# Optimization experiments

Hardware: AMD Instinct MI355X
Metric: run time of the kernel (lower is better)

The kernel has to match this reference:

```python
import jax, jax.numpy as jnp
import numpy as np

NBITS = 4
QN, QP = -(2 ** (NBITS - 1)), 2 ** (NBITS - 1) - 1  # -8, 7
NUM_HEADS = 12


def round_ste(x):
    # round_pass: straight-through estimator round
    return x + jax.lax.stop_gradient(jnp.round(x) - x)


def act3b(x, alpha, bias=0.0, signed=True):
    qn, qp = (-4.0, 3.0) if signed else (0.0, 7.0)
    return round_ste(jnp.clip((x + bias) / alpha, qn, qp))


def setup_inputs() -> dict:
    key = jax.random.key(0)
    ks = jax.random.split(key, 20)
    B, N, C, H = 32, 512, 768, NUM_HEADS
    hd = C // H
    u = lambda k, s: jax.random.uniform(k, s, jnp.float32, 0.05, 0.15)
    return {
        'x0': jax.random.normal(ks[0], (B, N, C), jnp.float32),
        'qkv_w': 0.02 * jax.random.normal(ks[1], (3 * C, C), jnp.float32),
        'qkv_alpha': u(ks[2], (3 * C,)),
        'qkv_bias': 0.02 * jax.random.normal(ks[3], (3 * C,), jnp.float32),
        'qkv_act_alpha': u(ks[4], (C,)),
        'proj_w': 0.02 * jax.random.normal(ks[5], (C, C), jnp.float32),
        'proj_alpha': u(ks[6], (C,)),
        'proj_bias': 0.02 * jax.random.normal(ks[7], (C,), jnp.float32),
        'proj_act_alpha': u(ks[8], (C,)),
        'normq_w': jax.random.uniform(ks[9], (hd,), jnp.float32, 0.8, 1.2),
        'normq_b': 0.01 * jax.random.normal(ks[10], (hd,), jnp.float32),
        'normk_w': jax.random.uniform(ks[11], (hd,), jnp.float32, 0.8, 1.2),
        'normk_b': 0.01 * jax.random.normal(ks[12], (hd,), jnp.float32),
        'qact_alpha': u(ks[13], (H,)),
        'kact_alpha': u(ks[14], (H,)),
        'vact_alpha': u(ks[15], (H,)),
        'attnact_alpha': u(ks[16], (H,)),
    }


def reference(x0, qkv_w, qkv_alpha, qkv_bias, qkv_act_alpha, proj_w, proj_alpha,
              proj_bias, proj_act_alpha, normq_w, normq_b, normk_w, normk_b,
              qact_alpha, kact_alpha, vact_alpha, attnact_alpha):
    B, N, C = x0.shape
    H = NUM_HEADS
    hd = C // H
    scale = hd ** -0.5

    # input activation quant (ActQ_v2, nbits=4)
    a_in = qkv_act_alpha.mean()
    x0_q = round_ste(jnp.clip(x0 / a_in, QN, QP))
    # kernel-wise 4-bit weight quant for qkv (no dequant here; scales folded later)
    w_q = round_ste(jnp.clip(qkv_w / qkv_alpha[:, None], QN, QP))
    qkv = x0_q @ w_q.T
    # integer-domain bias (truncated toward zero, like .int())
    qkv = qkv + jnp.trunc(qkv_bias / a_in / qkv_alpha)

    qkv = qkv.reshape(B, N, 3, H, hd).transpose(2, 0, 3, 1, 4)  # [3,B,H,N,hd]
    q0, k0, v0 = qkv[0], qkv[1], qkv[2]
    alpha3 = qkv_alpha.reshape(3, H, 1, hd)

    # fused scaled LayerNorm + 3-bit quant for q and k
    def norm_quant(x, ch_scale, nw, nb, act_a):
        xs = x * ch_scale  # [B,H,N,hd]
        centered = xs - xs.mean(-1, keepdims=True)
        std = jnp.std(xs, axis=-1, ddof=1, keepdims=True)
        return act3b(centered / (std + 1e-5), alpha=act_a / nw, bias=nb / nw)

    q2 = norm_quant(q0, alpha3[0], normq_w, normq_b, qact_alpha.mean())
    k2 = norm_quant(k0, alpha3[1], normk_w, normk_b, kact_alpha.mean())
    v2 = act3b(v0, alpha=vact_alpha.mean() / (a_in * alpha3[2]))

    # integer QK^T
    qk = jnp.einsum('bhqd,bhkd->bhqk', q2, k2)

    # base-2 softmax approximation
    div = 128.0
    sm_scale = scale * qact_alpha.mean() * kact_alpha.mean()
    e = jnp.trunc((1.0 / np.log(2)) * sm_scale * qk * div)
    attn_exp = jnp.exp2(jnp.round(e / div))
    attn = act3b(attn_exp / attn_exp.sum(-1, keepdims=True),
                 alpha=attnact_alpha.mean(), signed=False)

    # integer AV
    x1 = jnp.einsum('bhqk,bhkd->bhqd', attn, v2)
    x1 = x1.transpose(0, 2, 1, 3).reshape(B, N, C)
    x1_q = act3b(x1, alpha=proj_act_alpha.mean() / (attnact_alpha.mean() * vact_alpha.mean()))

    pw_q = round_ste(jnp.clip(proj_w / proj_alpha[:, None], QN, QP))
    out = (x1_q @ pw_q.T) * proj_alpha * proj_act_alpha.mean() + proj_bias
    return out
```

## Files before the change

kernel.cpp:

```cpp
#include <hip/hip_runtime.h>
#include <stdint.h>


#define BB 32
#define NN 512
#define CC 768
#define HH 12
#define HD 64
#define M_ROWS (BB * NN)
#define QKV_C (3 * CC)
#define KTA ((size_t)M_ROWS * 64)
#define KTB ((size_t)QKV_C * 64)
#define KTP ((size_t)CC * 64)

typedef int v4i __attribute__((ext_vector_type(4)));
typedef int v16i __attribute__((ext_vector_type(16)));

__device__ __forceinline__ float fadd(float a, float b) { return __fadd_rn(a, b); }
__device__ __forceinline__ float fmul(float a, float b) { return __fmul_rn(a, b); }
__device__ __forceinline__ float fdiv(float a, float b) { return __fdiv_rn(a, b); }
__device__ __forceinline__ float fsub(float a, float b) { return __fsub_rn(a, b); }

__device__ float np_sum_96(const float* a) {
  float r[8];
#pragma unroll
  for (int j = 0; j < 8; j++) r[j] = a[j];
  for (int i = 8; i < 96; i += 8)
#pragma unroll
    for (int j = 0; j < 8; j++) r[j] = fadd(r[j], a[i + j]);
  return fadd(fadd(fadd(r[0], r[1]), fadd(r[2], r[3])),
              fadd(fadd(r[4], r[5]), fadd(r[6], r[7])));
}

__device__ float np_mean_12(const float* a) {
  float r[8];
#pragma unroll
  for (int j = 0; j < 8; j++) r[j] = a[j];
  float res = fadd(fadd(fadd(r[0], r[1]), fadd(r[2], r[3])),
                   fadd(fadd(r[4], r[5]), fadd(r[6], r[7])));
  res = fadd(res, a[8]);
  res = fadd(res, a[9]);
  res = fadd(res, a[10]);
  res = fadd(res, a[11]);
  return fdiv(res, 12.0f);
}

__global__ void prep_kernel(const float* __restrict__ qkv_act_alpha,
                            const float* __restrict__ proj_act_alpha,
                            const float* __restrict__ qact_alpha,
                            const float* __restrict__ kact_alpha,
                            const float* __restrict__ vact_alpha,
                            const float* __restrict__ attnact_alpha,
                            const float* __restrict__ normq_w,
                            const float* __restrict__ normq_b,
                            const float* __restrict__ normk_w,
                            const float* __restrict__ normk_b,
                            const float* __restrict__ qkv_bias,
                            const float* __restrict__ qkv_alpha,
                            float* __restrict__ scal,
                            float* __restrict__ qparams,
                            float* __restrict__ biasq) {
  __shared__ float s_scal[8];
  __shared__ float chunk[16];
  int tid = threadIdx.x;
  if (tid < 8) chunk[tid] = np_sum_96(qkv_act_alpha + 96 * tid);
  else if (tid < 16) chunk[tid] = np_sum_96(proj_act_alpha + 96 * (tid - 8));
  if (tid == 16) s_scal[1] = np_mean_12(qact_alpha);
  if (tid == 17) s_scal[2] = np_mean_12(kact_alpha);
  if (tid == 18) s_scal[3] = np_mean_12(vact_alpha);
  if (tid == 19) s_scal[4] = np_mean_12(attnact_alpha);
  __syncthreads();
  if (tid == 0) {
    float s0 = fadd(fadd(chunk[0], chunk[1]), fadd(chunk[2], chunk[3]));
    float s1 = fadd(fadd(chunk[4], chunk[5]), fadd(chunk[6], chunk[7]));
    s_scal[0] = fdiv(fadd(s0, s1), 768.0f);
    float p0 = fadd(fadd(chunk[8], chunk[9]), fadd(chunk[10], chunk[11]));
    float p1 = fadd(fadd(chunk[12], chunk[13]), fadd(chunk[14], chunk[15]));
    s_scal[5] = fdiv(fadd(p0, p1), 768.0f);
  }
  __syncthreads();
  if (tid < 6) scal[tid] = s_scal[tid];
  if (tid < 64) {
    qparams[tid]       = fdiv(s_scal[1], normq_w[tid]);
    qparams[64 + tid]  = fdiv(normq_b[tid], normq_w[tid]);
    qparams[128 + tid] = fdiv(s_scal[2], normk_w[tid]);
    qparams[192 + tid] = fdiv(normk_b[tid], normk_w[tid]);
  }
  float a_in = s_scal[0];
  for (int c = tid; c < QKV_C; c += blockDim.x)
    biasq[c] = truncf(fdiv(fdiv(qkv_bias[c], a_in), qkv_alpha[c]));
}

__device__ __forceinline__ size_t fragaddr(int row, int b) {
  return (size_t)(row & ~31) * 64 + ((b >> 4) * 512 + (row & 31) * 16 + (b & 15));
}

__global__ void quant_x0_kernel(const float* __restrict__ x0,
                                const float* __restrict__ scal,
                                int8_t* __restrict__ x0q, int total4) {
  int i = blockIdx.x * blockDim.x + threadIdx.x;
  if (i >= total4) return;
  float a_in = scal[0];
  float4 v = ((const float4*)x0)[i];
  char4 o;
  o.x = (int8_t)rintf(fminf(fmaxf(fdiv(v.x, a_in), -8.f), 7.f));
  o.y = (int8_t)rintf(fminf(fmaxf(fdiv(v.y, a_in), -8.f), 7.f));
  o.z = (int8_t)rintf(fminf(fmaxf(fdiv(v.z, a_in), -8.f), 7.f));
  o.w = (int8_t)rintf(fminf(fmaxf(fdiv(v.w, a_in), -8.f), 7.f));
  int seq = i / 192;
  int kp = (i - seq * 192) * 4;
  int b = kp & 63;
  *(char4*)(x0q + (size_t)(kp >> 6) * KTA + fragaddr(seq, b)) = o;
}

__global__ void quant_w_kernel(const float* __restrict__ w,
                               const float* __restrict__ alpha,
                               int8_t* __restrict__ wq, int rows, int total) {
  int i = blockIdx.x * blockDim.x + threadIdx.x;
  if (i >= total) return;
  int row = i / CC;
  int k = i - row * CC;
  float t = fminf(fmaxf(fdiv(w[i], alpha[row]), -8.f), 7.f);
  wq[(size_t)(k >> 6) * ((size_t)rows * 64) + fragaddr(row, k)] =
      (int8_t)rintf(t);
}

__global__ __launch_bounds__(256, 5) void gemm_qkv_kernel(
    const int8_t* __restrict__ Aq, const int8_t* __restrict__ Wq,
    const float* __restrict__ biasq, const float* __restrict__ scal,
    const float* __restrict__ qkv_alpha, const float* __restrict__ qparams,
    int8_t* __restrict__ q2, int8_t* __restrict__ k2,
    int8_t* __restrict__ v2f) {
  __shared__ __align__(16) int8_t packT[4][3072];

  const int L = blockIdx.x;
  const int xcd = L & 7, s = L >> 3;
  const int rb = xcd + 8 * (s / 36);
  const int g = s % 36;
  const int tid = threadIdx.x;
  const int w = tid >> 6, lane = tid & 63;
  const int l31 = lane & 31, hi = lane >> 5;
  const int sec = g / HH, head = g % HH;
  const int col0 = g * 64;
  const int b_idx = rb >> 2, nbase = (rb & 3) * 128;
  const int w32 = w * 32;
  const size_t bh = (size_t)b_idx * HH + head;

  v16i acc0 = (v16i)(0), acc1 = (v16i)(0);

  const int8_t* pa = Aq + (size_t)(rb * 128 + w32) * 64 + hi * 512 + l31 * 16;
  const int8_t* pb = Wq + (size_t)col0 * 64 + hi * 512 + l31 * 16;

  if (sec < 2) {
    v4i Aa = *(const v4i*)(pa);
    v4i Ab = *(const v4i*)(pa + 1024);
    v4i B0a = *(const v4i*)(pb);
    v4i B0b = *(const v4i*)(pb + 1024);
    v4i B1a = *(const v4i*)(pb + 2048);
    v4i B1b = *(const v4i*)(pb + 3072);
#pragma unroll 1
    for (int kt = 0; kt < 11; kt++) {
      const int8_t* npa = pa + (size_t)(kt + 1) * KTA;
      const int8_t* npb = pb + (size_t)(kt + 1) * KTB;
      v4i nAa = *(const v4i*)(npa);
      v4i nAb = *(const v4i*)(npa + 1024);
      v4i nB0a = *(const v4i*)(npb);
      v4i nB0b = *(const v4i*)(npb + 1024);
      v4i nB1a = *(const v4i*)(npb + 2048);
      v4i nB1b = *(const v4i*)(npb + 3072);
      acc0 = __builtin_amdgcn_mfma_i32_32x32x32_i8(B0a, Aa, acc0, 0, 0, 0);
      acc1 = __builtin_amdgcn_mfma_i32_32x32x32_i8(B1a, Aa, acc1, 0, 0, 0);
      acc0 = __builtin_amdgcn_mfma_i32_32x32x32_i8(B0b, Ab, acc0, 0, 0, 0);
      acc1 = __builtin_amdgcn_mfma_i32_32x32x32_i8(B1b, Ab, acc1, 0, 0, 0);
      Aa = nAa; Ab = nAb; B0a = nB0a; B0b = nB0b; B1a = nB1a; B1b = nB1b;
    }
    acc0 = __builtin_amdgcn_mfma_i32_32x32x32_i8(B0a, Aa, acc0, 0, 0, 0);
    acc1 = __builtin_amdgcn_mfma_i32_32x32x32_i8(B1a, Aa, acc1, 0, 0, 0);
    acc0 = __builtin_amdgcn_mfma_i32_32x32x32_i8(B0b, Ab, acc0, 0, 0, 0);
    acc1 = __builtin_amdgcn_mfma_i32_32x32x32_i8(B1b, Ab, acc1, 0, 0, 0);
    float xs[2][16];
#pragma unroll
    for (int i = 0; i < 2; i++)
#pragma unroll
      for (int b = 0; b < 4; b++) {
        int cg = col0 + 32 * i + 8 * b + 4 * hi;
        float4 bqv = *(const float4*)(biasq + cg);
        float4 alv = *(const float4*)(qkv_alpha + cg);
        const float* bqp = (const float*)&bqv;
        const float* alp = (const float*)&alv;
#pragma unroll
        for (int c = 0; c < 4; c++) {
          int av = (i == 0) ? acc0[4 * b + c] : acc1[4 * b + c];
          xs[i][4 * b + c] = fmul(fadd((float)av, bqp[c]), alp[c]);
        }
      }
    float rc[4];
#pragma unroll
    for (int c = 0; c < 4; c++) rc[c] = xs[0][c];
#pragma unroll
    for (int b = 1; b < 4; b++)
#pragma unroll
      for (int c = 0; c < 4; c++) rc[c] = fadd(rc[c], xs[0][4 * b + c]);
#pragma unroll
    for (int b = 0; b < 4; b++)
#pragma unroll
      for (int c = 0; c < 4; c++) rc[c] = fadd(rc[c], xs[1][4 * b + c]);
    float Ls = fadd(fadd(rc[0], rc[1]), fadd(rc[2], rc[3]));
    float Rs = __shfl_xor(Ls, 32, 64);
    float mn = fdiv(fadd(Ls, Rs), 64.0f);
    float vc[4];
#pragma unroll
    for (int c = 0; c < 4; c++) {
      float d = fsub(xs[0][c], mn);
      vc[c] = fmul(d, d);
    }
#pragma unroll
    for (int b = 1; b < 4; b++)
#pragma unroll
      for (int c = 0; c < 4; c++) {
        float d = fsub(xs[0][4 * b + c], mn);
        vc[c] = fadd(vc[c], fmul(d, d));
      }
#pragma unroll
    for (int b = 0; b < 4; b++)
#pragma unroll
      for (int c = 0; c < 4; c++) {
        float d = fsub(xs[1][4 * b + c], mn);
        vc[c] = fadd(vc[c], fmul(d, d));
      }
    float Lv = fadd(fadd(vc[0], vc[1]), fadd(vc[2], vc[3]));
    float Rv = __shfl_xor(Lv, 32, 64);
    float var = fdiv(fadd(Lv, Rv), 63.0f);
    float den = fadd(__fsqrt_rn(var), 1e-5f);
    const float* ap = qparams + (sec == 0 ? 0 : 128);
#pragma unroll
    for (int i = 0; i < 2; i++)
#pragma unroll
      for (int b = 0; b < 4; b++) {
        int cin = 32 * i + 8 * b + 4 * hi;
        float4 a4 = *(const float4*)(ap + cin);
        float4 b4 = *(const float4*)(ap + 64 + cin);
        const float* a4p = (const float*)&a4;
        const float* b4p = (const float*)&b4;
        uint32_t pk = 0;
#pragma unroll
        for (int c = 0; c < 4; c++) {
          float xn = fdiv(fsub(xs[i][4 * b + c], mn), den);
          float t = fdiv(fadd(xn, b4p[c]), a4p[c]);
          t = fminf(fmaxf(t, -4.f), 3.f);
          pk |= ((uint32_t)(uint8_t)(int8_t)rintf(t)) << (8 * c);
        }
        *(uint32_t*)&packT[w][l31 * 80 + cin] = pk;
      }
    asm volatile("s_waitcnt lgkmcnt(0)" ::: "memory");
    int8_t* dst = (sec == 0) ? q2 : k2;
    size_t rowbase = bh * NN + nbase + w32;
#pragma unroll
    for (int c = 0; c < 2; c++) {
      int id = lane + 64 * c;
      int row = id >> 2, off = (id & 3) * 16;
      int4 ov = *(const int4*)&packT[w][row * 80 + off];
      *(int4*)(dst + (rowbase + row) * 64 + off) = ov;
    }
  } else {
    v4i Aa = *(const v4i*)(pa);
    v4i Ab = *(const v4i*)(pa + 1024);
    v4i B0a = *(const v4i*)(pb);
    v4i B0b = *(const v4i*)(pb + 1024);
    v4i B1a = *(const v4i*)(pb + 2048);
    v4i B1b = *(const v4i*)(pb + 3072);
#pragma unroll 1
    for (int kt = 0; kt < 11; kt++) {
      const int8_t* npa = pa + (size_t)(kt + 1) * KTA;
      const int8_t* npb = pb + (size_t)(kt + 1) * KTB;
      v4i nAa = *(const v4i*)(npa);
      v4i nAb = *(const v4i*)(npa + 1024);
      v4i nB0a = *(const v4i*)(npb);
      v4i nB0b = *(const v4i*)(npb + 1024);
      v4i nB1a = *(const v4i*)(npb + 2048);
      v4i nB1b = *(const v4i*)(npb + 3072);
      acc0 = __builtin_amdgcn_mfma_i32_32x32x32_i8(Aa, B0a, acc0, 0, 0, 0);
      acc1 = __builtin_amdgcn_mfma_i32_32x32x32_i8(Aa, B1a, acc1, 0, 0, 0);
      acc0 = __builtin_amdgcn_mfma_i32_32x32x32_i8(Ab, B0b, acc0, 0, 0, 0);
      acc1 = __builtin_amdgcn_mfma_i32_32x32x32_i8(Ab, B1b, acc1, 0, 0, 0);
      Aa = nAa; Ab = nAb; B0a = nB0a; B0b = nB0b; B1a = nB1a; B1b = nB1b;
    }
    acc0 = __builtin_amdgcn_mfma_i32_32x32x32_i8(Aa, B0a, acc0, 0, 0, 0);
    acc1 = __builtin_amdgcn_mfma_i32_32x32x32_i8(Aa, B1a, acc1, 0, 0, 0);
    acc0 = __builtin_amdgcn_mfma_i32_32x32x32_i8(Ab, B0b, acc0, 0, 0, 0);
    acc1 = __builtin_amdgcn_mfma_i32_32x32x32_i8(Ab, B1b, acc1, 0, 0, 0);
    const float a_in = scal[0], vact = scal[3];
#pragma unroll
    for (int sj = 0; sj < 2; sj++) {
      int cg = col0 + 32 * sj + l31;
      float bq = biasq[cg];
      float va = fdiv(vact, fmul(a_in, qkv_alpha[cg]));
      int dloc = 32 * sj + l31;
#pragma unroll
      for (int b = 0; b < 4; b++) {
        uint32_t pk = 0;
#pragma unroll
        for (int c = 0; c < 4; c++) {
          int av = (sj == 0) ? acc0[4 * b + c] : acc1[4 * b + c];
          float vint = fadd((float)av, bq);
          float t = fminf(fmaxf(fdiv(vint, va), -4.f), 3.f);
          pk |= ((uint32_t)(uint8_t)(int8_t)rintf(t)) << (8 * c);
        }
        *(uint32_t*)&packT[w][dloc * 48 + 8 * b + 4 * hi] = pk;
      }
    }
    asm volatile("s_waitcnt lgkmcnt(0)" ::: "memory");
#pragma unroll
    for (int c = 0; c < 2; c++) {
      int id = lane + 64 * c;
      int row = id >> 1, off = (id & 1) * 16;
      int4 ov = *(const int4*)&packT[w][row * 48 + off];
      int n0 = nbase + w32 + off;
      *(int4*)(v2f + (size_t)bh * 32768 + ((n0 >> 6) * 4096) +
               ((row >> 4) * 1024) + ((row & 15) * 64) +
               (((n0 >> 4) & 3) * 16)) = ov;
    }
  }
}

__global__ __launch_bounds__(256) void attn_kernel(
    const int8_t* __restrict__ q2, const int8_t* __restrict__ k2,
    const int8_t* __restrict__ v2f, const float* __restrict__ scal,
    int8_t* __restrict__ x1q) {
  __shared__ __align__(16) int8_t At[64][80];

  const int L = blockIdx.x;
  const int xcd = L & 7, s = L >> 3;
  const int bh = xcd + 8 * (s >> 3);
  const int qt = s & 7;
  const int tid = threadIdx.x;
  const int w = tid >> 6, lane = tid & 63, quad = lane >> 4, c16 = lane & 15;
  const int sr = tid >> 2, scol = (tid & 3) << 4;
  const float attnm = scal[4];
  const float coef =
      fmul(1.4426950408889634f, fmul(fmul(0.125f, scal[1]), scal[2]));
  const float coef128 = fmul(coef, 128.f);
  const size_t base = (size_t)bh * NN * HD;

  const int8_t* kptr = k2 + base + (size_t)c16 * 64 + quad * 16;
  const int8_t* vptr = v2f + base + (size_t)c16 * 64 + quad * 16;
  v4i qf = *(const v4i*)(q2 + base + (size_t)(qt * 64 + 16 * w + c16) * 64 +
                         quad * 16);

  uint32_t mpack[8][4];
  float Srow = 0.f;
  v4i kfr[4];
#pragma unroll
  for (int f = 0; f < 4; f++)
    kfr[f] = *(const v4i*)(kptr + f * 1024);
#pragma unroll
  for (int kt = 0; kt < 8; kt++) {
    float psum = 0.f;
#pragma unroll
    for (int f = 0; f < 4; f++) {
      v4i kf = kfr[f];
      if (kt < 7)
        kfr[f] = *(const v4i*)(kptr + (kt + 1) * 4096 + f * 1024);
      v4i d2 = (v4i){0, 0, 0, 0};
      d2 = __builtin_amdgcn_mfma_i32_16x16x64_i8(kf, qf, d2, 0, 0, 0);
      uint32_t pk = 0;
#pragma unroll
      for (int r = 0; r < 4; r++) {
        float e = truncf(fmul(coef128, (float)d2[r]));
        int mi = (int)rintf(fmul(e, 0.0078125f));
        psum = fadd(psum, ldexpf(1.0f, mi));
        pk |= ((uint32_t)(uint8_t)(int8_t)mi) << (8 * r);
      }
      mpack[kt][f] = pk;
    }
    psum = fadd(psum, __shfl_xor(psum, 16, 64));
    psum = fadd(psum, __shfl_xor(psum, 32, 64));
    Srow = fadd(Srow, psum);
  }
  const float u = fdiv(fdiv(1.0f, Srow), attnm);

  v4i xacc[4];
#pragma unroll
  for (int s2 = 0; s2 < 4; s2++) xacc[s2] = (v4i){0, 0, 0, 0};
  v4i vfr[4];
#pragma unroll
  for (int s2 = 0; s2 < 4; s2++)
    vfr[s2] = *(const v4i*)(vptr + s2 * 1024);

#pragma unroll
  for (int kt = 0; kt < 8; kt++) {
#pragma unroll
    for (int f = 0; f < 4; f++) {
      uint32_t pk = mpack[kt][f];
      uint32_t wpk = 0;
#pragma unroll
      for (int r = 0; r < 4; r++) {
        int mi = (int)(int8_t)(pk >> (8 * r));
        float t = fminf(ldexpf(u, mi), 7.f);
        wpk |= ((uint32_t)(uint8_t)(int8_t)rintf(t)) << (8 * r);
      }
      *(uint32_t*)&At[16 * w + c16][16 * f + 4 * quad] = wpk;
    }
    asm volatile("s_waitcnt lgkmcnt(0)" ::: "memory");
    v4i af = *(const v4i*)&At[16 * w + c16][quad * 16];
#pragma unroll
    for (int s2 = 0; s2 < 4; s2++) {
      v4i vf = vfr[s2];
      if (kt < 7)
        vfr[s2] = *(const v4i*)(vptr + (kt + 1) * 4096 + s2 * 1024);
      xacc[s2] = __builtin_amdgcn_mfma_i32_16x16x64_i8(vf, af, xacc[s2], 0, 0, 0);
    }
  }

  const float pa = fdiv(scal[5], fmul(attnm, scal[3]));
#pragma unroll
  for (int s2 = 0; s2 < 4; s2++) {
    uint32_t pack = 0;
#pragma unroll
    for (int r = 0; r < 4; r++) {
      float t = fminf(fmaxf(fdiv((float)xacc[s2][r], pa), -4.f), 3.f);
      pack |= ((uint32_t)(uint8_t)(int8_t)rintf(t)) << (8 * r);
    }
    *(uint32_t*)&At[16 * w + c16][16 * s2 + 4 * quad] = pack;
  }
  __syncthreads();
  int4 ov = *(const int4*)&At[sr][scol];
  *(int4*)(x1q + ((size_t)bh * NN + qt * 64 + sr) * HD + scol) = ov;
}

__global__ __launch_bounds__(256, 5) void gemm_proj_kernel(
    const int8_t* __restrict__ x1q, const int8_t* __restrict__ Wq,
    const float* __restrict__ proj_alpha, const float* __restrict__ proj_bias,
    const float* __restrict__ scal, float* __restrict__ out) {
  const int L = blockIdx.x;
  const int xcd = L & 7, s = L >> 3;
  const int rb = xcd + 8 * (s / 12);
  const int g = s % 12;
  const int tid = threadIdx.x;
  const int w = tid >> 6, lane = tid & 63;
  const int l31 = lane & 31, hi = lane >> 5;
  const int col0 = g * 64;
  const int b_idx = rb >> 2, nbase = (rb & 3) * 128;
  const int w32 = w * 32;

  v16i acc0 = (v16i)(0), acc1 = (v16i)(0);

  const int8_t* pa =
      x1q + ((size_t)b_idx * HH * NN + nbase + w32 + l31) * 64 + hi * 16;
  const int8_t* pb = Wq + (size_t)col0 * 64 + hi * 512 + l31 * 16;
  const size_t KTX = (size_t)NN * 64;

  v4i Aa = *(const v4i*)(pa);
  v4i Ab = *(const v4i*)(pa + 32);
  v4i B0a = *(const v4i*)(pb);
  v4i B0b = *(const v4i*)(pb + 1024);
  v4i B1a = *(const v4i*)(pb + 2048);
  v4i B1b = *(const v4i*)(pb + 3072);
#pragma unroll 1
  for (int kt = 0; kt < 11; kt++) {
    const int8_t* npa = pa + (size_t)(kt + 1) * KTX;
    const int8_t* npb = pb + (size_t)(kt + 1) * KTP;
    v4i nAa = *(const v4i*)(npa);
    v4i nAb = *(const v4i*)(npa + 32);
    v4i nB0a = *(const v4i*)(npb);
    v4i nB0b = *(const v4i*)(npb + 1024);
    v4i nB1a = *(const v4i*)(npb + 2048);
    v4i nB1b = *(const v4i*)(npb + 3072);
    acc0 = __builtin_amdgcn_mfma_i32_32x32x32_i8(B0a, Aa, acc0, 0, 0, 0);
    acc1 = __builtin_amdgcn_mfma_i32_32x32x32_i8(B1a, Aa, acc1, 0, 0, 0);
    acc0 = __builtin_amdgcn_mfma_i32_32x32x32_i8(B0b, Ab, acc0, 0, 0, 0);
    acc1 = __builtin_amdgcn_mfma_i32_32x32x32_i8(B1b, Ab, acc1, 0, 0, 0);
    Aa = nAa; Ab = nAb; B0a = nB0a; B0b = nB0b; B1a = nB1a; B1b = nB1b;
  }
  acc0 = __builtin_amdgcn_mfma_i32_32x32x32_i8(B0a, Aa, acc0, 0, 0, 0);
  acc1 = __builtin_amdgcn_mfma_i32_32x32x32_i8(B1a, Aa, acc1, 0, 0, 0);
  acc0 = __builtin_amdgcn_mfma_i32_32x32x32_i8(B0b, Ab, acc0, 0, 0, 0);
  acc1 = __builtin_amdgcn_mfma_i32_32x32x32_i8(B1b, Ab, acc1, 0, 0, 0);

  const float pact = scal[5];
  const int m = rb * 128 + w32 + l31;
#pragma unroll
  for (int i = 0; i < 2; i++)
#pragma unroll
    for (int b = 0; b < 4; b++) {
      int colb = col0 + 32 * i + 8 * b + 4 * hi;
      float4 al = *(const float4*)(proj_alpha + colb);
      float4 bi = *(const float4*)(proj_bias + colb);
      const float* alp = (const float*)&al;
      const float* bip = (const float*)&bi;
      float4 o;
      float* op = (float*)&o;
#pragma unroll
      for (int c = 0; c < 4; c++) {
        int av = (i == 0) ? acc0[4 * b + c] : acc1[4 * b + c];
        op[c] = fadd(fmul(fmul((float)av, alp[c]), pact), bip[c]);
      }
      *(float4*)(out + (size_t)m * CC + colb) = o;
    }
}

extern "C" void kernel_launch(void* const* d_in, const int* in_sizes, int n_in,
                              void* d_out, int out_size, void* d_ws,
                              size_t ws_size, hipStream_t stream) {
  const float* x0 = (const float*)d_in[0];
  const float* qkv_w = (const float*)d_in[1];
  const float* qkv_alpha = (const float*)d_in[2];
  const float* qkv_bias = (const float*)d_in[3];
  const float* qkv_act_alpha = (const float*)d_in[4];
  const float* proj_w = (const float*)d_in[5];
  const float* proj_alpha = (const float*)d_in[6];
  const float* proj_bias = (const float*)d_in[7];
  const float* proj_act_alpha = (const float*)d_in[8];
  const float* normq_w = (const float*)d_in[9];
  const float* normq_b = (const float*)d_in[10];
  const float* normk_w = (const float*)d_in[11];
  const float* normk_b = (const float*)d_in[12];
  const float* qact_alpha = (const float*)d_in[13];
  const float* kact_alpha = (const float*)d_in[14];
  const float* vact_alpha = (const float*)d_in[15];
  const float* attnact_alpha = (const float*)d_in[16];

  char* ws = (char*)d_ws;
  size_t off = 0;
  auto alloc = [&](size_t bytes) -> char* {
    char* p = ws + off;
    off += (bytes + 255) & ~(size_t)255;
    return p;
  };
  float* scal = (float*)alloc(64 * 4);
  float* qparams = (float*)alloc(256 * 4);
  float* biasq = (float*)alloc(QKV_C * 4);
  int8_t* x0q = (int8_t*)alloc((size_t)M_ROWS * CC);
  int8_t* wq = (int8_t*)alloc((size_t)QKV_C * CC);
  int8_t* pwq = (int8_t*)alloc((size_t)CC * CC);
  int8_t* q2 = (int8_t*)alloc((size_t)BB * HH * NN * HD);
  int8_t* k2 = (int8_t*)alloc((size_t)BB * HH * NN * HD);
  int8_t* v2f = (int8_t*)alloc((size_t)BB * HH * NN * HD);
  int8_t* x1q = (int8_t*)alloc((size_t)M_ROWS * CC);

  prep_kernel<<<1, 256, 0, stream>>>(qkv_act_alpha, proj_act_alpha, qact_alpha,
                                     kact_alpha, vact_alpha, attnact_alpha,
                                     normq_w, normq_b, normk_w, normk_b,
                                     qkv_bias, qkv_alpha, scal, qparams, biasq);

  int total4 = M_ROWS * CC / 4;
  quant_x0_kernel<<<(total4 + 255) / 256, 256, 0, stream>>>(x0, scal, x0q,
                                                            total4);
  quant_w_kernel<<<(QKV_C * CC + 255) / 256, 256, 0, stream>>>(
      qkv_w, qkv_alpha, wq, QKV_C, QKV_C * CC);
  quant_w_kernel<<<(CC * CC + 255) / 256, 256, 0, stream>>>(
      proj_w, proj_alpha, pwq, CC, CC * CC);

  gemm_qkv_kernel<<<36 * (M_ROWS / 128), 256, 0, stream>>>(
      x0q, wq, biasq, scal, qkv_alpha, qparams, q2, k2, v2f);

  attn_kernel<<<(NN / 64) * (BB * HH), 256, 0, stream>>>(q2, k2, v2f, scal,
                                                         x1q);

  gemm_proj_kernel<<<12 * (M_ROWS / 128), 256, 0, stream>>>(
      x1q, pwq, proj_alpha, proj_bias, scal, (float*)d_out);
}
```

Measured before the change: 298.5 us.

## Double the row tile per wave in both int8 GEMMs to 64x64

Each wave in the QKV and projection GEMMs now computes a 64-row by 64-column tile with four MFMA accumulators instead of 32x64 with two. Each B fragment is reused across two A fragments, which cuts global B loads per MFMA, and the grids shrink by half to match. The epilogues loop over the two row halves. In exchange, register pressure roughly doubles, so the occupancy hint of 5 is dropped and fewer workgroups can be resident. The smaller grid may also reduce load balance across CUs.

```diff
diff --git a/kernel.cpp b/kernel.cpp
--- a/kernel.cpp
+++ b/kernel.cpp
@@ -125,7 +125,7 @@
       (int8_t)rintf(t);
 }
 
-__global__ __launch_bounds__(256, 5) void gemm_qkv_kernel(
+__global__ __launch_bounds__(256) void gemm_qkv_kernel(
     const int8_t* __restrict__ Aq, const int8_t* __restrict__ Wq,
     const float* __restrict__ biasq, const float* __restrict__ scal,
     const float* __restrict__ qkv_alpha, const float* __restrict__ qparams,
@@ -142,18 +142,21 @@
   const int l31 = lane & 31, hi = lane >> 5;
   const int sec = g / HH, head = g % HH;
   const int col0 = g * 64;
-  const int b_idx = rb >> 2, nbase = (rb & 3) * 128;
-  const int w32 = w * 32;
+  const int b_idx = rb >> 1, nbase = (rb & 1) * 256;
+  const int w64 = w * 64;
   const size_t bh = (size_t)b_idx * HH + head;
 
-  v16i acc0 = (v16i)(0), acc1 = (v16i)(0);
-
-  const int8_t* pa = Aq + (size_t)(rb * 128 + w32) * 64 + hi * 512 + l31 * 16;
+  v16i acc00 = (v16i)(0), acc01 = (v16i)(0);
+  v16i acc10 = (v16i)(0), acc11 = (v16i)(0);
+
+  const int8_t* pa = Aq + (size_t)(rb * 256 + w64) * 64 + hi * 512 + l31 * 16;
   const int8_t* pb = Wq + (size_t)col0 * 64 + hi * 512 + l31 * 16;
 
   if (sec < 2) {
-    v4i Aa = *(const v4i*)(pa);
-    v4i Ab = *(const v4i*)(pa + 1024);
+    v4i A0a = *(const v4i*)(pa);
+    v4i A0b = *(const v4i*)(pa + 1024);
+    v4i A1a = *(const v4i*)(pa + 2048);
+    v4i A1b = *(const v4i*)(pa + 3072);
     v4i B0a = *(const v4i*)(pb);
     v4i B0b = *(const v4i*)(pb + 1024);
     v4i B1a = *(const v4i*)(pb + 2048);
@@ -162,109 +165,130 @@
     for (int kt = 0; kt < 11; kt++) {
       const int8_t* npa = pa + (size_t)(kt + 1) * KTA;
       const int8_t* npb = pb + (size_t)(kt + 1) * KTB;
-      v4i nAa = *(const v4i*)(npa);
-      v4i nAb = *(const v4i*)(npa + 1024);
+      v4i nA0a = *(const v4i*)(npa);
+      v4i nA0b = *(const v4i*)(npa + 1024);
+      v4i nA1a = *(const v4i*)(npa + 2048);
+      v4i nA1b = *(const v4i*)(npa + 3072);
       v4i nB0a = *(const v4i*)(npb);
       v4i nB0b = *(const v4i*)(npb + 1024);
       v4i nB1a = *(const v4i*)(npb + 2048);
       v4i nB1b = *(const v4i*)(npb + 3072);
-      acc0 = __builtin_amdgcn_mfma_i32_32x32x32_i8(B0a, Aa, acc0, 0, 0, 0);
-      acc1 = __builtin_amdgcn_mfma_i32_32x32x32_i8(B1a, Aa, acc1, 0, 0, 0);
-      acc0 = __builtin_amdgcn_mfma_i32_32x32x32_i8(B0b, Ab, acc0, 0, 0, 0);
-      acc1 = __builtin_amdgcn_mfma_i32_32x32x32_i8(B1b, Ab, acc1, 0, 0, 0);
-      Aa = nAa; Ab = nAb; B0a = nB0a; B0b = nB0b; B1a = nB1a; B1b = nB1b;
-    }
-    acc0 = __builtin_amdgcn_mfma_i32_32x32x32_i8(B0a, Aa, acc0, 0, 0, 0);
-    acc1 = __builtin_amdgcn_mfma_i32_32x32x32_i8(B1a, Aa, acc1, 0, 0, 0);
-    acc0 = __builtin_amdgcn_mfma_i32_32x32x32_i8(B0b, Ab, acc0, 0, 0, 0);
-    acc1 = __builtin_amdgcn_mfma_i32_32x32x32_i8(B1b, Ab, acc1, 0, 0, 0);
-    float xs[2][16];
-#pragma unroll
-    for (int i = 0; i < 2; i++)
-#pragma unroll
-      for (int b = 0; b < 4; b++) {
-        int cg = col0 + 32 * i + 8 * b + 4 * hi;
-        float4 bqv = *(const float4*)(biasq + cg);
-        float4 alv = *(const float4*)(qkv_alpha + cg);
-        const float* bqp = (const float*)&bqv;
-        const float* alp = (const float*)&alv;
+      acc00 = __builtin_amdgcn_mfma_i32_32x32x32_i8(B0a, A0a, acc00, 0, 0, 0);
+      acc01 = __builtin_amdgcn_mfma_i32_32x32x32_i8(B1a, A0a, acc01, 0, 0, 0);
+      acc10 = __builtin_amdgcn_mfma_i32_32x32x32_i8(B0a, A1a, acc10, 0, 0, 0);
+      acc11 = __builtin_amdgcn_mfma_i32_32x32x32_i8(B1a, A1a, acc11, 0, 0, 0);
+      acc00 = __builtin_amdgcn_mfma_i32_32x32x32_i8(B0b, A0b, acc00, 0, 0, 0);
+      acc01 = __builtin_amdgcn_mfma_i32_32x32x32_i8(B1b, A0b, acc01, 0, 0, 0);
+      acc10 = __builtin_amdgcn_mfma_i32_32x32x32_i8(B0b, A1b, acc10, 0, 0, 0);
+      acc11 = __builtin_amdgcn_mfma_i32_32x32x32_i8(B1b, A1b, acc11, 0, 0, 0);
+      A0a = nA0a; A0b = nA0b; A1a = nA1a; A1b = nA1b;
+      B0a = nB0a; B0b = nB0b; B1a = nB1a; B1b = nB1b;
+    }
+    acc00 = __builtin_amdgcn_mfma_i32_32x32x32_i8(B0a, A0a, acc00, 0, 0, 0);
+    acc01 = __builtin_amdgcn_mfma_i32_32x32x32_i8(B1a, A0a, acc01, 0, 0, 0);
+    acc10 = __builtin_amdgcn_mfma_i32_32x32x32_i8(B0a, A1a, acc10, 0, 0, 0);
+    acc11 = __builtin_amdgcn_mfma_i32_32x32x32_i8(B1a, A1a, acc11, 0, 0, 0);
+    acc00 = __builtin_amdgcn_mfma_i32_32x32x32_i8(B0b, A0b, acc00, 0, 0, 0);
+    acc01 = __builtin_amdgcn_mfma_i32_32x32x32_i8(B1b, A0b, acc01, 0, 0, 0);
+    acc10 = __builtin_amdgcn_mfma_i32_32x32x32_i8(B0b, A1b, acc10, 0, 0, 0);
+    acc11 = __builtin_amdgcn_mfma_i32_32x32x32_i8(B1b, A1b, acc11, 0, 0, 0);
+
+    const float* ap = qparams + (sec == 0 ? 0 : 128);
+    int8_t* dst = (sec == 0) ? q2 : k2;
+#pragma unroll
+    for (int p = 0; p < 2; p++) {
+      float xs[2][16];
+#pragma unroll
+      for (int i = 0; i < 2; i++)
+#pragma unroll
+        for (int b = 0; b < 4; b++) {
+          int cg = col0 + 32 * i + 8 * b + 4 * hi;
+          float4 bqv = *(const float4*)(biasq + cg);
+          float4 alv = *(const float4*)(qkv_alpha + cg);
+          const float* bqp = (const float*)&bqv;
+          const float* alp = (const float*)&alv;
+#pragma unroll
+          for (int c = 0; c < 4; c++) {
+            int av;
+            if (p == 0)
+              av = (i == 0) ? acc00[4 * b + c] : acc01[4 * b + c];
+            else
+              av = (i == 0) ? acc10[4 * b + c] : acc11[4 * b + c];
+            xs[i][4 * b + c] = fmul(fadd((float)av, bqp[c]), alp[c]);
+          }
+        }
+      float rc[4];
+#pragma unroll
+      for (int c = 0; c < 4; c++) rc[c] = xs[0][c];
+#pragma unroll
+      for (int b = 1; b < 4; b++)
+#pragma unroll
+        for (int c = 0; c < 4; c++) rc[c] = fadd(rc[c], xs[0][4 * b + c]);
+#pragma unroll
+      for (int b = 0; b < 4; b++)
+#pragma unroll
+        for (int c = 0; c < 4; c++) rc[c] = fadd(rc[c], xs[1][4 * b + c]);
+      float Ls = fadd(fadd(rc[0], rc[1]), fadd(rc[2], rc[3]));
+      float Rs = __shfl_xor(Ls, 32, 64);
+      float mn = fdiv(fadd(Ls, Rs), 64.0f);
+      float vc[4];
+#pragma unroll
+      for (int c = 0; c < 4; c++) {
+        float d = fsub(xs[0][c], mn);
+        vc[c] = fmul(d, d);
+      }
+#pragma unroll
+      for (int b = 1; b < 4; b++)
 #pragma unroll
         for (int c = 0; c < 4; c++) {
-          int av = (i == 0) ? acc0[4 * b + c] : acc1[4 * b + c];
-          xs[i][4 * b + c] = fmul(fadd((float)av, bqp[c]), alp[c]);
+          float d = fsub(xs[0][4 * b + c], mn);
+          vc[c] = fadd(vc[c], fmul(d, d));
         }
+#pragma unroll
+      for (int b = 0; b < 4; b++)
+#pragma unroll
+        for (int c = 0; c < 4; c++) {
+          float d = fsub(xs[1][4 * b + c], mn);
+          vc[c] = fadd(vc[c], fmul(d, d));
+        }
+      float Lv = fadd(fadd(vc[0], vc[1]), fadd(vc[2], vc[3]));
+      float Rv = __shfl_xor(Lv, 32, 64);
+      float var = fdiv(fadd(Lv, Rv), 63.0f);
+      float den = fadd(__fsqrt_rn(var), 1e-5f);
+#pragma unroll
+      for (int i = 0; i < 2; i++)
+#pragma unroll
+        for (int b = 0; b < 4; b++) {
+          int cin = 32 * i + 8 * b + 4 * hi;
+          float4 a4 = *(const float4*)(ap + cin);
+          float4 b4 = *(const float4*)(ap + 64 + cin);
+          const float* a4p = (const float*)&a4;
+          const float* b4p = (const float*)&b4;
+          uint32_t pk = 0;
+#pragma unroll
+          for (int c = 0; c < 4; c++) {
+            float xn = fdiv(fsub(xs[i][4 * b + c], mn), den);
+            float t = fdiv(fadd(xn, b4p[c]), a4p[c]);
+            t = fminf(fmaxf(t, -4.f), 3.f);
+            pk |= ((uint32_t)(uint8_t)(int8_t)rintf(t)) << (8 * c);
+          }
+          *(uint32_t*)&packT[w][l31 * 80 + cin] = pk;
+        }
+      asm volatile("s_waitcnt lgkmcnt(0)" ::: "memory");
+      size_t rowbase = bh * NN + nbase + w64 + p * 32;
+#pragma unroll
+      for (int c = 0; c < 2; c++) {
+        int id = lane + 64 * c;
+        int row = id >> 2, off = (id & 3) * 16;
+        int4 ov = *(const int4*)&packT[w][row * 80 + off];
+        *(int4*)(dst + (rowbase + row) * 64 + off) = ov;
       }
-    float rc[4];
-#pragma unroll
-    for (int c = 0; c < 4; c++) rc[c] = xs[0][c];
-#pragma unroll
-    for (int b = 1; b < 4; b++)
-#pragma unroll
-      for (int c = 0; c < 4; c++) rc[c] = fadd(rc[c], xs[0][4 * b + c]);
-#pragma unroll
-    for (int b = 0; b < 4; b++)
-#pragma unroll
-      for (int c = 0; c < 4; c++) rc[c] = fadd(rc[c], xs[1][4 * b + c]);
-    float Ls = fadd(fadd(rc[0], rc[1]), fadd(rc[2], rc[3]));
-    float Rs = __shfl_xor(Ls, 32, 64);
-    float mn = fdiv(fadd(Ls, Rs), 64.0f);
-    float vc[4];
-#pragma unroll
-    for (int c = 0; c < 4; c++) {
-      float d = fsub(xs[0][c], mn);
-      vc[c] = fmul(d, d);
-    }
-#pragma unroll
-    for (int b = 1; b < 4; b++)
-#pragma unroll
-      for (int c = 0; c < 4; c++) {
-        float d = fsub(xs[0][4 * b + c], mn);
-        vc[c] = fadd(vc[c], fmul(d, d));
-      }
-#pragma unroll
-    for (int b = 0; b < 4; b++)
-#pragma unroll
-      for (int c = 0; c < 4; c++) {
-        float d = fsub(xs[1][4 * b + c], mn);
-        vc[c] = fadd(vc[c], fmul(d, d));
-      }
-    float Lv = fadd(fadd(vc[0], vc[1]), fadd(vc[2], vc[3]));
-    float Rv = __shfl_xor(Lv, 32, 64);
-    float var = fdiv(fadd(Lv, Rv), 63.0f);
-    float den = fadd(__fsqrt_rn(var), 1e-5f);
-    const float* ap = qparams + (sec == 0 ? 0 : 128);
-#pragma unroll
-    for (int i = 0; i < 2; i++)
-#pragma unroll
-      for (int b = 0; b < 4; b++) {
-        int cin = 32 * i + 8 * b + 4 * hi;
-        float4 a4 = *(const float4*)(ap + cin);
-        float4 b4 = *(const float4*)(ap + 64 + cin);
-        const float* a4p = (const float*)&a4;
-        const float* b4p = (const float*)&b4;
-        uint32_t pk = 0;
-#pragma unroll
-        for (int c = 0; c < 4; c++) {
-          float xn = fdiv(fsub(xs[i][4 * b + c], mn), den);
-          float t = fdiv(fadd(xn, b4p[c]), a4p[c]);
-          t = fminf(fmaxf(t, -4.f), 3.f);
-          pk |= ((uint32_t)(uint8_t)(int8_t)rintf(t)) << (8 * c);
-        }
-        *(uint32_t*)&packT[w][l31 * 80 + cin] = pk;
-      }
-    asm volatile("s_waitcnt lgkmcnt(0)" ::: "memory");
-    int8_t* dst = (sec == 0) ? q2 : k2;
-    size_t rowbase = bh * NN + nbase + w32;
-#pragma unroll
-    for (int c = 0; c < 2; c++) {
-      int id = lane + 64 * c;
-      int row = id >> 2, off = (id & 3) * 16;
-      int4 ov = *(const int4*)&packT[w][row * 80 + off];
-      *(int4*)(dst + (rowbase + row) * 64 + off) = ov;
     }
   } else {
-    v4i Aa = *(const v4i*)(pa);
-    v4i Ab = *(const v4i*)(pa + 1024);
+    v4i A0a = *(const v4i*)(pa);
+    v4i A0b = *(const v4i*)(pa + 1024);
+    v4i A1a = *(const v4i*)(pa + 2048);
+    v4i A1b = *(const v4i*)(pa + 3072);
     v4i B0a = *(const v4i*)(pb);
     v4i B0b = *(const v4i*)(pb + 1024);
     v4i B1a = *(const v4i*)(pb + 2048);
@@ -273,52 +297,71 @@
     for (int kt = 0; kt < 11; kt++) {
       const int8_t* npa = pa + (size_t)(kt + 1) * KTA;
       const int8_t* npb = pb + (size_t)(kt + 1) * KTB;
-      v4i nAa = *(const v4i*)(npa);
-      v4i nAb = *(const v4i*)(npa + 1024);
+      v4i nA0a = *(const v4i*)(npa);
+      v4i nA0b = *(const v4i*)(npa + 1024);
+      v4i nA1a = *(const v4i*)(npa + 2048);
+      v4i nA1b = *(const v4i*)(npa + 3072);
       v4i nB0a = *(const v4i*)(npb);
       v4i nB0b = *(const v4i*)(npb + 1024);
       v4i nB1a = *(const v4i*)(npb + 2048);
       v4i nB1b = *(const v4i*)(npb + 3072);
-      acc0 = __builtin_amdgcn_mfma_i32_32x32x32_i8(Aa, B0a, acc0, 0, 0, 0);
-      acc1 = __builtin_amdgcn_mfma_i32_32x32x32_i8(Aa, B1a, acc1, 0, 0, 0);
-      acc0 = __builtin_amdgcn_mfma_i32_32x32x32_i8(Ab, B0b, acc0, 0, 0, 0);
-      acc1 = __builtin_amdgcn_mfma_i32_32x32x32_i8(Ab, B1b, acc1, 0, 0, 0);
-      Aa = nAa; Ab = nAb; B0a = nB0a; B0b = nB0b; B1a = nB1a; B1b = nB1b;
-    }
-    acc0 = __builtin_amdgcn_mfma_i32_32x32x32_i8(Aa, B0a, acc0, 0, 0, 0);
-    acc1 = __builtin_amdgcn_mfma_i32_32x32x32_i8(Aa, B1a, acc1, 0, 0, 0);
-    acc0 = __builtin_amdgcn_mfma_i32_32x32x32_i8(Ab, B0b, acc0, 0, 0, 0);
-    acc1 = __builtin_amdgcn_mfma_i32_32x32x32_i8(Ab, B1b, acc1, 0, 0, 0);
+      acc00 = __builtin_amdgcn_mfma_i32_32x32x32_i8(A0a, B0a, acc00, 0, 0, 0);
+      acc01 = __builtin_amdgcn_mfma_i32_32x32x32_i8(A0a, B1a, acc01, 0, 0, 0);
+      acc10 = __builtin_amdgcn_mfma_i32_32x32x32_i8(A1a, B0a, acc10, 0, 0, 0);
+      acc11 = __builtin_amdgcn_mfma_i32_32x32x32_i8(A1a, B1a, acc11, 0, 0, 0);
+      acc00 = __builtin_amdgcn_mfma_i32_32x32x32_i8(A0b, B0b, acc00, 0, 0, 0);
+      acc01 = __builtin_amdgcn_mfma_i32_32x32x32_i8(A0b, B1b, acc01, 0, 0, 0);
+      acc10 = __builtin_amdgcn_mfma_i32_32x32x32_i8(A1b, B0b, acc10, 0, 0, 0);
+      acc11 = __builtin_amdgcn_mfma_i32_32x32x32_i8(A1b, B1b, acc11, 0, 0, 0);
+      A0a = nA0a; A0b = nA0b; A1a = nA1a; A1b = nA1b;
+      B0a = nB0a; B0b = nB0b; B1a = nB1a; B1b = nB1b;
+    }
+    acc00 = __builtin_amdgcn_mfma_i32_32x32x32_i8(A0a, B0a, acc00, 0, 0, 0);
+    acc01 = __builtin_amdgcn_mfma_i32_32x32x32_i8(A0a, B1a, acc01, 0, 0, 0);
+    acc10 = __builtin_amdgcn_mfma_i32_32x32x32_i8(A1a, B0a, acc10, 0, 0, 0);
+    acc11 = __builtin_amdgcn_mfma_i32_32x32x32_i8(A1a, B1a, acc11, 0, 0, 0);
+    acc00 = __builtin_amdgcn_mfma_i32_32x32x32_i8(A0b, B0b, acc00, 0, 0, 0);
+    acc01 = __builtin_amdgcn_mfma_i32_32x32x32_i8(A0b, B1b, acc01, 0, 0, 0);
+    acc10 = __builtin_amdgcn_mfma_i32_32x32x32_i8(A1b, B0b, acc10, 0, 0, 0);
+    acc11 = __builtin_amdgcn_mfma_i32_32x32x32_i8(A1b, B1b, acc11, 0, 0, 0);
+
     const float a_in = scal[0], vact = scal[3];
 #pragma unroll
-    for (int sj = 0; sj < 2; sj++) {
-      int cg = col0 + 32 * sj + l31;
-      float bq = biasq[cg];
-      float va = fdiv(vact, fmul(a_in, qkv_alpha[cg]));
-      int dloc = 32 * sj + l31;
-#pragma unroll
-      for (int b = 0; b < 4; b++) {
-        uint32_t pk = 0;
-#pragma unroll
-        for (int c = 0; c < 4; c++) {
-          int av = (sj == 0) ? acc0[4 * b + c] : acc1[4 * b + c];
-          float vint = fadd((float)av, bq);
-          float t = fminf(fmaxf(fdiv(vint, va), -4.f), 3.f);
-          pk |= ((uint32_t)(uint8_t)(int8_t)rintf(t)) << (8 * c);
+    for (int p = 0; p < 2; p++) {
+#pragma unroll
+      for (int sj = 0; sj < 2; sj++) {
+        int cg = col0 + 32 * sj + l31;
+        float bq = biasq[cg];
+        float va = fdiv(vact, fmul(a_in, qkv_alpha[cg]));
+        int dloc = 32 * sj + l31;
+#pragma unroll
+        for (int b = 0; b < 4; b++) {
+          uint32_t pk = 0;
+#pragma unroll
+          for (int c = 0; c < 4; c++) {
+            int av;
+            if (p == 0)
+              av = (sj == 0) ? acc00[4 * b + c] : acc01[4 * b + c];
+            else
+              av = (sj == 0) ? acc10[4 * b + c] : acc11[4 * b + c];
+            float vint = fadd((float)av, bq);
+            float t = fminf(fmaxf(fdiv(vint, va), -4.f), 3.f);
+            pk |= ((uint32_t)(uint8_t)(int8_t)rintf(t)) << (8 * c);
+          }
+          *(uint32_t*)&packT[w][dloc * 48 + 8 * b + 4 * hi] = pk;
         }
-        *(uint32_t*)&packT[w][dloc * 48 + 8 * b + 4 * hi] = pk;
       }
-    }
-    asm volatile("s_waitcnt lgkmcnt(0)" ::: "memory");
-#pragma unroll
-    for (int c = 0; c < 2; c++) {
-      int id = lane + 64 * c;
-      int row = id >> 1, off = (id & 1) * 16;
-      int4 ov = *(const int4*)&packT[w][row * 48 + off];
-      int n0 = nbase + w32 + off;
-      *(int4*)(v2f + (size_t)bh * 32768 + ((n0 >> 6) * 4096) +
-               ((row >> 4) * 1024) + ((row & 15) * 64) +
-               (((n0 >> 4) & 3) * 16)) = ov;
+      asm volatile("s_waitcnt lgkmcnt(0)" ::: "memory");
+#pragma unroll
+      for (int c = 0; c < 2; c++) {
+        int id = lane + 64 * c;
+        int row = id >> 1, off = (id & 1) * 16;
+        int4 ov = *(const int4*)&packT[w][row * 48 + off];
+        int n0 = nbase + w64 + p * 32 + off;
+        *(int4*)(v2f + (size_t)bh * 32768 + ((n0 >> 6) * 4096) +
+                 ((row >> 4) * 1024) + ((row & 15) * 64) +
+                 (((n0 >> 4) & 3) * 16)) = ov;
+      }
     }
   }
 }
@@ -428,7 +471,7 @@
   *(int4*)(x1q + ((size_t)bh * NN + qt * 64 + sr) * HD + scol) = ov;
 }
 
-__global__ __launch_bounds__(256, 5) void gemm_proj_kernel(
+__global__ __launch_bounds__(256) void gemm_proj_kernel(
     const int8_t* __restrict__ x1q, const int8_t* __restrict__ Wq,
     const float* __restrict__ proj_alpha, const float* __restrict__ proj_bias,
     const float* __restrict__ scal, float* __restrict__ out) {
@@ -440,18 +483,21 @@
   const int w = tid >> 6, lane = tid & 63;
   const int l31 = lane & 31, hi = lane >> 5;
   const int col0 = g * 64;
-  const int b_idx = rb >> 2, nbase = (rb & 3) * 128;
-  const int w32 = w * 32;
-
-  v16i acc0 = (v16i)(0), acc1 = (v16i)(0);
+  const int b_idx = rb >> 1, nbase = (rb & 1) * 256;
+  const int w64 = w * 64;
+
+  v16i acc00 = (v16i)(0), acc01 = (v16i)(0);
+  v16i acc10 = (v16i)(0), acc11 = (v16i)(0);
 
   const int8_t* pa =
-      x1q + ((size_t)b_idx * HH * NN + nbase + w32 + l31) * 64 + hi * 16;
+      x1q + ((size_t)b_idx * HH * NN + nbase + w64 + l31) * 64 + hi * 16;
   const int8_t* pb = Wq + (size_t)col0 * 64 + hi * 512 + l31 * 16;
   const size_t KTX = (size_t)NN * 64;
 
-  v4i Aa = *(const v4i*)(pa);
-  v4i Ab = *(const v4i*)(pa + 32);
+  v4i A0a = *(const v4i*)(pa);
+  v4i A0b = *(const v4i*)(pa + 32);
+  v4i A1a = *(const v4i*)(pa + 2048);
+  v4i A1b = *(const v4i*)(pa + 2048 + 32);
   v4i B0a = *(const v4i*)(pb);
   v4i B0b = *(const v4i*)(pb + 1024);
   v4i B1a = *(const v4i*)(pb + 2048);
@@ -460,43 +506,61 @@
   for (int kt = 0; kt < 11; kt++) {
     const int8_t* npa = pa + (size_t)(kt + 1) * KTX;
     const int8_t* npb = pb + (size_t)(kt + 1) * KTP;
-    v4i nAa = *(const v4i*)(npa);
-    v4i nAb = *(const v4i*)(npa + 32);
+    v4i nA0a = *(const v4i*)(npa);
+    v4i nA0b = *(const v4i*)(npa + 32);
+    v4i nA1a = *(const v4i*)(npa + 2048);
+    v4i nA1b = *(const v4i*)(npa + 2048 + 32);
     v4i nB0a = *(const v4i*)(npb);
     v4i nB0b = *(const v4i*)(npb + 1024);
     v4i nB1a = *(const v4i*)(npb + 2048);
     v4i nB1b = *(const v4i*)(npb + 3072);
-    acc0 = __builtin_amdgcn_mfma_i32_32x32x32_i8(B0a, Aa, acc0, 0, 0, 0);
-    acc1 = __builtin_amdgcn_mfma_i32_32x32x32_i8(B1a, Aa, acc1, 0, 0, 0);
-    acc0 = __builtin_amdgcn_mfma_i32_32x32x32_i8(B0b, Ab, acc0, 0, 0, 0);
-    acc1 = __builtin_amdgcn_mfma_i32_32x32x32_i8(B1b, Ab, acc1, 0, 0, 0);
-    Aa = nAa; Ab = nAb; B0a = nB0a; B0b = nB0b; B1a = nB1a; B1b = nB1b;
-  }
-  acc0 = __builtin_amdgcn_mfma_i32_32x32x32_i8(B0a, Aa, acc0, 0, 0, 0);
-  acc1 = __builtin_amdgcn_mfma_i32_32x32x32_i8(B1a, Aa, acc1, 0, 0, 0);
-  acc0 = __builtin_amdgcn_mfma_i32_32x32x32_i8(B0b, Ab, acc0, 0, 0, 0);
-  acc1 = __builtin_amdgcn_mfma_i32_32x32x32_i8(B1b, Ab, acc1, 0, 0, 0);
+    acc00 = __builtin_amdgcn_mfma_i32_32x32x32_i8(B0a, A0a, acc00, 0, 0, 0);
+    acc01 = __builtin_amdgcn_mfma_i32_32x32x32_i8(B1a, A0a, acc01, 0, 0, 0);
+    acc10 = __builtin_amdgcn_mfma_i32_32x32x32_i8(B0a, A1a, acc10, 0, 0, 0);
+    acc11 = __builtin_amdgcn_mfma_i32_32x32x32_i8(B1a, A1a, acc11, 0, 0, 0);
+    acc00 = __builtin_amdgcn_mfma_i32_32x32x32_i8(B0b, A0b, acc00, 0, 0, 0);
+    acc01 = __builtin_amdgcn_mfma_i32_32x32x32_i8(B1b, A0b, acc01, 0, 0, 0);
+    acc10 = __builtin_amdgcn_mfma_i32_32x32x32_i8(B0b, A1b, acc10, 0, 0, 0);
+    acc11 = __builtin_amdgcn_mfma_i32_32x32x32_i8(B1b, A1b, acc11, 0, 0, 0);
+    A0a = nA0a; A0b = nA0b; A1a = nA1a; A1b = nA1b;
+    B0a = nB0a; B0b = nB0b; B1a = nB1a; B1b = nB1b;
+  }
+  acc00 = __builtin_amdgcn_mfma_i32_32x32x32_i8(B0a, A0a, acc00, 0, 0, 0);
+  acc01 = __builtin_amdgcn_mfma_i32_32x32x32_i8(B1a, A0a, acc01, 0, 0, 0);
+  acc10 = __builtin_amdgcn_mfma_i32_32x32x32_i8(B0a, A1a, acc10, 0, 0, 0);
+  acc11 = __builtin_amdgcn_mfma_i32_32x32x32_i8(B1a, A1a, acc11, 0, 0, 0);
+  acc00 = __builtin_amdgcn_mfma_i32_32x32x32_i8(B0b, A0b, acc00, 0, 0, 0);
+  acc01 = __builtin_amdgcn_mfma_i32_32x32x32_i8(B1b, A0b, acc01, 0, 0, 0);
+  acc10 = __builtin_amdgcn_mfma_i32_32x32x32_i8(B0b, A1b, acc10, 0, 0, 0);
+  acc11 = __builtin_amdgcn_mfma_i32_32x32x32_i8(B1b, A1b, acc11, 0, 0, 0);
 
   const float pact = scal[5];
-  const int m = rb * 128 + w32 + l31;
-#pragma unroll
-  for (int i = 0; i < 2; i++)
-#pragma unroll
-    for (int b = 0; b < 4; b++) {
-      int colb = col0 + 32 * i + 8 * b + 4 * hi;
-      float4 al = *(const float4*)(proj_alpha + colb);
-      float4 bi = *(const float4*)(proj_bias + colb);
-      const float* alp = (const float*)&al;
-      const float* bip = (const float*)&bi;
-      float4 o;
-      float* op = (float*)&o;
-#pragma unroll
-      for (int c = 0; c < 4; c++) {
-        int av = (i == 0) ? acc0[4 * b + c] : acc1[4 * b + c];
-        op[c] = fadd(fmul(fmul((float)av, alp[c]), pact), bip[c]);
+#pragma unroll
+  for (int p = 0; p < 2; p++) {
+    const int m = rb * 256 + w64 + p * 32 + l31;
+#pragma unroll
+    for (int i = 0; i < 2; i++)
+#pragma unroll
+      for (int b = 0; b < 4; b++) {
+        int colb = col0 + 32 * i + 8 * b + 4 * hi;
+        float4 al = *(const float4*)(proj_alpha + colb);
+        float4 bi = *(const float4*)(proj_bias + colb);
+        const float* alp = (const float*)&al;
+        const float* bip = (const float*)&bi;
+        float4 o;
+        float* op = (float*)&o;
+#pragma unroll
+        for (int c = 0; c < 4; c++) {
+          int av;
+          if (p == 0)
+            av = (i == 0) ? acc00[4 * b + c] : acc01[4 * b + c];
+          else
+            av = (i == 0) ? acc10[4 * b + c] : acc11[4 * b + c];
+          op[c] = fadd(fmul(fmul((float)av, alp[c]), pact), bip[c]);
+        }
+        *(float4*)(out + (size_t)m * CC + colb) = o;
       }
-      *(float4*)(out + (size_t)m * CC + colb) = o;
-    }
+  }
 }
 
 extern "C" void kernel_launch(void* const* d_in, const int* in_sizes, int n_in,
@@ -551,12 +615,12 @@
   quant_w_kernel<<<(CC * CC + 255) / 256, 256, 0, stream>>>(
       proj_w, proj_alpha, pwq, CC, CC * CC);
 
-  gemm_qkv_kernel<<<36 * (M_ROWS / 128), 256, 0, stream>>>(
+  gemm_qkv_kernel<<<36 * (M_ROWS / 256), 256, 0, stream>>>(
       x0q, wq, biasq, scal, qkv_alpha, qparams, q2, k2, v2f);
 
   attn_kernel<<<(NN / 64) * (BB * HH), 256, 0, stream>>>(q2, k2, v2f, scal,
                                                          x1q);
 
-  gemm_proj_kernel<<<12 * (M_ROWS / 128), 256, 0, stream>>>(
+  gemm_proj_kernel<<<12 * (M_ROWS / 256), 256, 0, stream>>>(
       x1q, pwq, proj_alpha, proj_bias, scal, (float*)d_out);
 }
```

After: 291.6 us. 2.3% less time.
